# Kernel tuning notes

Hardware: AMD Instinct MI355X
Metric: run time of the kernel (lower is better)

The kernel has to match this reference:

```python
import jax, jax.numpy as jnp
import numpy as np

B, S, I, H, T = 64, 512, 300, 512, 25


def setup_inputs() -> dict:
    key = jax.random.key(0)
    ks = jax.random.split(key, 16)
    kH = 1.0 / np.sqrt(H)
    x = jax.random.normal(ks[0], (B, S, I), jnp.float32)
    lengths = jax.random.randint(ks[1], (B,), S // 2, S + 1)
    attention_mask = (jnp.arange(S)[None, :] < lengths[:, None]).astype(jnp.int32)
    raw = jax.random.randint(ks[2], (B, S), 0, T)
    labels = jnp.where(attention_mask > 0, raw, -100).astype(jnp.int32)
    u = lambda k, sh: jax.random.uniform(k, sh, jnp.float32, -kH, kH)
    return {
        'input_ids': x,
        'W_ih_f': u(ks[3], (4 * H, I)), 'W_hh_f': u(ks[4], (4 * H, H)), 'b_f': u(ks[5], (4 * H,)),
        'W_ih_b': u(ks[6], (4 * H, I)), 'W_hh_b': u(ks[7], (4 * H, H)), 'b_b': u(ks[8], (4 * H,)),
        'Wc': u(ks[9], (T, 2 * H)), 'bc': u(ks[10], (T,)),
        'crf_start': jax.random.uniform(ks[11], (T,), jnp.float32, -0.1, 0.1),
        'crf_end': jax.random.uniform(ks[12], (T,), jnp.float32, -0.1, 0.1),
        'crf_trans': jax.random.uniform(ks[13], (T, T), jnp.float32, -0.1, 0.1),
        'attention_mask': attention_mask,
        'labels': labels,
    }


def _lstm_scan(x, mask, W_ih, W_hh, b):
    # x: [B,S,I], mask: [B,S] bool. PyTorch gate order i,f,g,o. Masked steps
    # freeze (h,c) and emit zeros, matching pack_padded/pad_packed semantics.
    Bb, Ss, _ = x.shape
    Hh = W_hh.shape[1]
    pre = jnp.einsum('bsi,gi->sbg', x, W_ih) + b  # [S,B,4H] input projection
    mt = jnp.moveaxis(mask, 1, 0)                 # [S,B]

    def step(carry, xs):
        h, c = carry
        p_t, m_t = xs
        gates = p_t + h @ W_hh.T
        i, f, g, o = jnp.split(gates, 4, axis=-1)
        c_new = jax.nn.sigmoid(f) * c + jax.nn.sigmoid(i) * jnp.tanh(g)
        h_new = jax.nn.sigmoid(o) * jnp.tanh(c_new)
        m = m_t[:, None]
        return (jnp.where(m, h_new, h), jnp.where(m, c_new, c)), jnp.where(m, h_new, 0.0)

    h0 = jnp.zeros((Bb, Hh), x.dtype)
    _, ys = jax.lax.scan(step, (h0, h0), (pre, mt))
    return jnp.moveaxis(ys, 0, 1)  # [B,S,H]


def _crf_nll_token_mean(em, tags, mask, start, end, trans):
    # pytorch-crf log-likelihood with reduction='token_mean'; returns -llh.
    Bb, Ss, Tt = em.shape
    mf = mask.astype(em.dtype)
    batch = jnp.arange(Bb)
    emit = jnp.take_along_axis(em, tags[..., None], axis=2)[..., 0]  # [B,S]
    num = start[tags[:, 0]] + emit[:, 0]
    tr = trans[tags[:, :-1], tags[:, 1:]]  # [B,S-1]
    num = num + jnp.sum(mf[:, 1:] * (tr + emit[:, 1:]), axis=1)
    last_idx = jnp.sum(mask.astype(jnp.int32), axis=1) - 1
    num = num + end[tags[batch, last_idx]]

    em_t = jnp.moveaxis(em[:, 1:], 1, 0)    # [S-1,B,T]
    mk_t = jnp.moveaxis(mask[:, 1:], 1, 0)  # [S-1,B]

    def step(score, xs):
        e_t, m_t = xs
        nxt = jax.nn.logsumexp(score[:, :, None] + trans[None] + e_t[:, None, :], axis=1)
        return jnp.where(m_t[:, None], nxt, score), None

    score0 = start[None] + em[:, 0]
    score, _ = jax.lax.scan(step, score0, (em_t, mk_t))
    denom = jax.nn.logsumexp(score + end[None], axis=1)
    llh = num - denom
    return -(jnp.sum(llh) / jnp.sum(mf))


def _crf_decode(em, mask, start, end, trans):
    Bb, Ss, Tt = em.shape
    em_t = jnp.moveaxis(em[:, 1:], 1, 0)
    mk_t = jnp.moveaxis(mask[:, 1:], 1, 0)
    idT = jnp.arange(Tt)
    batch = jnp.arange(Bb)

    def step(score, xs):
        e_t, m_t = xs
        cand = score[:, :, None] + trans[None]     # [B,T,T]
        best_prev = jnp.argmax(cand, axis=1)       # [B,T]
        best = jnp.max(cand, axis=1) + e_t
        m = m_t[:, None]
        return jnp.where(m, best, score), jnp.where(m, best_prev, idT[None, :])

    score0 = start[None] + em[:, 0]
    score, hist = jax.lax.scan(step, score0, (em_t, mk_t))  # hist [S-1,B,T]
    last_tag = jnp.argmax(score + end[None], axis=1)        # [B]

    def back(tag, xs):
        h_t, m_t = xs
        tag2 = jnp.where(m_t, h_t[batch, tag], tag)
        return tag2, tag2

    _, prev_tags = jax.lax.scan(back, last_tag, (hist, mk_t), reverse=True)  # [S-1,B]
    tags = jnp.concatenate([prev_tags, last_tag[None]], axis=0)  # [S,B]
    return jnp.moveaxis(tags, 0, 1)  # [B,S]


def _forward(input_ids, W_ih_f, W_hh_f, b_f, W_ih_b, W_hh_b, b_b, Wc, bc,
             crf_start, crf_end, crf_trans, attention_mask, labels):
    mask = attention_mask > 0
    lengths = jnp.sum(attention_mask, axis=1)  # [B]
    # forward direction
    h_f = _lstm_scan(input_ids, mask, W_ih_f, W_hh_f, b_f)
    # backward direction: reverse each sequence within its valid length
    t_idx = jnp.arange(input_ids.shape[1])[None, :]
    rev = jnp.where(t_idx < lengths[:, None], lengths[:, None] - 1 - t_idx, t_idx)
    x_rev = jnp.take_along_axis(input_ids, rev[:, :, None], axis=1)
    m_rev = jnp.take_along_axis(mask, rev, axis=1)
    h_b_rev = _lstm_scan(x_rev, m_rev, W_ih_b, W_hh_b, b_b)
    h_b = jnp.take_along_axis(h_b_rev, rev[:, :, None], axis=1)  # rev is an involution on the valid prefix
    seq = jnp.concatenate([h_f, h_b], axis=-1)  # [B,S,2H]; dropout = identity (eval)
    logits = seq @ Wc.T + bc                    # [B,S,T]
    # re-pack tokens with labels >= 0 to the front (stable), as the torch loop does
    valid = labels >= 0
    order = jnp.argsort(jnp.logical_not(valid), axis=1, stable=True)
    new_logits = jnp.take_along_axis(logits, order[:, :, None], axis=1)
    new_labels = jnp.take_along_axis(labels, order, axis=1)
    pred_mask = jnp.take_along_axis(valid, order, axis=1)
    active = jnp.where(pred_mask, new_labels, 0)
    loss = _crf_nll_token_mean(new_logits, active, pred_mask, crf_start, crf_end, crf_trans)
    tags = _crf_decode(new_logits, pred_mask, crf_start, crf_end, crf_trans)
    return loss, logits, tags, pred_mask


def reference(input_ids, W_ih_f, W_hh_f, b_f, W_ih_b, W_hh_b, b_b, Wc, bc,
              crf_start, crf_end, crf_trans, attention_mask, labels):
    return _forward(input_ids, W_ih_f, W_hh_f, b_f, W_ih_b, W_hh_b, b_b, Wc, bc,
                    crf_start, crf_end, crf_trans, attention_mask, labels)
```

## Files before the change

kernel.cpp:

```cpp
#include <hip/hip_runtime.h>
#include <math.h>

#define B_ 64
#define S_ 512
#define I_ 300
#define H_ 512
#define T_ 25

typedef short bf16x8 __attribute__((ext_vector_type(8)));
typedef float f32x4  __attribute__((ext_vector_type(4)));

__host__ __device__ __forceinline__ int kmap(int l, int j) {
    return 16 * (j >> 2) + 4 * ((l >> 4) & 3) + (j & 3);
}

static constexpr size_t SZ_XBF_S = (size_t)S_ * 2 * 2 * 4 * 5 * 2 * 64 * 8;
static constexpr size_t OFS_XBF  = 0;
static constexpr size_t OFS_WHF  = OFS_XBF + SZ_XBF_S / 2;
static constexpr size_t SZ_WHF_S = (size_t)2 * 128 * 2 * 8 * 2 * 64 * 8;
static constexpr size_t OFS_WXF  = OFS_WHF + SZ_WHF_S / 2;
static constexpr size_t SZ_WXF_S = (size_t)2 * 128 * 2 * 5 * 2 * 64 * 8;
static constexpr size_t OFS_YF   = OFS_WXF + SZ_WXF_S / 2;
static constexpr size_t SZ_Y     = (size_t)S_ * H_ * B_;
static constexpr size_t OFS_YB   = OFS_YF + SZ_Y;
static constexpr size_t SZ_L     = (size_t)B_ * S_ * T_;
static constexpr size_t OFS_L1   = OFS_YB + SZ_Y;
static constexpr size_t OFS_L2   = OFS_L1 + SZ_L;
static constexpr size_t OFS_LEN  = OFS_L2 + SZ_L;
static constexpr size_t OFS_LLH  = OFS_LEN + 64;
static constexpr size_t OFS_FLG  = OFS_LLH + 64;

static constexpr size_t OFF_LOGITS = 1;
static constexpr size_t OFF_TAGS   = 1 + SZ_L;
static constexpr size_t OFF_MASK   = OFF_TAGS + (size_t)B_ * S_;

__global__ void k_lengths(const int* __restrict__ am, int* __restrict__ len) {
    int b = threadIdx.x;
    int sum = 0;
    for (int s = 0; s < S_; ++s) sum += am[b * S_ + s];
    len[b] = sum;
}

__global__ void k_zero(float* __restrict__ p, int n) {
    int idx = blockIdx.x * 256 + threadIdx.x;
    if (idx < n) p[idx] = 0.f;
}

__global__ void k_prep_hfrag(const float* __restrict__ whhf,
                             const float* __restrict__ whhb,
                             short* __restrict__ hf) {
    for (size_t idx = (size_t)blockIdx.x * 256 + threadIdx.x; idx < SZ_WHF_S;
         idx += (size_t)gridDim.x * 256) {
        int j = (int)(idx & 7); size_t t = idx >> 3;
        int l = (int)(t & 63); t >>= 6;
        int hilo = (int)(t & 1); t >>= 1;
        int kt = (int)(t & 7); t >>= 3;
        int kh = (int)(t & 1); t >>= 1;
        int ug = (int)(t & 127); t >>= 7;
        int dir = (int)t;
        int m = l & 15;
        int row = (m & 3) * H_ + ug * 4 + (m >> 2);
        int k = kh * 256 + kt * 32 + kmap(l, j);
        float w = (dir ? whhb : whhf)[(size_t)row * H_ + k];
        unsigned u32 = __float_as_uint(w);
        float hi_f = __uint_as_float(u32 & 0xffff0000u);
        hf[idx] = hilo ? (short)(__float_as_uint(w - hi_f) >> 16)
                       : (short)(u32 >> 16);
    }
}

__global__ void k_prep_xfrag(const float* __restrict__ wihf,
                             const float* __restrict__ wihb,
                             short* __restrict__ xf) {
    for (size_t idx = (size_t)blockIdx.x * 256 + threadIdx.x; idx < SZ_WXF_S;
         idx += (size_t)gridDim.x * 256) {
        int j = (int)(idx & 7); size_t t = idx >> 3;
        int l = (int)(t & 63); t >>= 6;
        int hilo = (int)(t & 1); t >>= 1;
        int kt = (int)(t % 5); t /= 5;
        int kh = (int)(t & 1); t >>= 1;
        int ug = (int)(t & 127); t >>= 7;
        int dir = (int)t;
        int m = l & 15;
        int row = (m & 3) * H_ + ug * 4 + (m >> 2);
        int k = kh * 160 + kt * 32 + kmap(l, j);
        float w = 0.f;
        if (k < I_) w = (dir ? wihb : wihf)[(size_t)row * I_ + k];
        unsigned u32 = __float_as_uint(w);
        float hi_f = __uint_as_float(u32 & 0xffff0000u);
        xf[idx] = hilo ? (short)(__float_as_uint(w - hi_f) >> 16)
                       : (short)(u32 >> 16);
    }
}

__global__ void k_prep_xb(const float* __restrict__ x, const int* __restrict__ len,
                          short* __restrict__ xb) {
    for (size_t idx = (size_t)blockIdx.x * 256 + threadIdx.x; idx < SZ_XBF_S;
         idx += (size_t)gridDim.x * 256) {
        int j = (int)(idx & 7); size_t t = idx >> 3;
        int l = (int)(t & 63); t >>= 6;
        int hilo = (int)(t & 1); t >>= 1;
        int kt = (int)(t % 5); t /= 5;
        int nt = (int)(t & 3); t >>= 2;
        int kh = (int)(t & 1); t >>= 1;
        int dir = (int)(t & 1); t >>= 1;
        int s = (int)t;
        int b = nt * 16 + (l & 15);
        int k = kh * 160 + kt * 32 + kmap(l, j);
        float v = 0.f;
        if (k < I_) {
            int src = s;
            if (dir) { int L = len[b]; src = (s < L) ? (L - 1 - s) : s; }
            v = x[((size_t)b * S_ + src) * I_ + k];
        }
        unsigned u32 = __float_as_uint(v);
        float hi_f = __uint_as_float(u32 & 0xffff0000u);
        xb[idx] = hilo ? (short)(__float_as_uint(v - hi_f) >> 16)
                       : (short)(u32 >> 16);
    }
}

__global__ __launch_bounds__(512, 2) void k_scan(
    const short* __restrict__ whf, const short* __restrict__ wxf,
    const short* __restrict__ xbf,
    float* yf, float* ybr,
    const float* __restrict__ bf, const float* __restrict__ bb,
    const int* __restrict__ len, int* __restrict__ flg)
{
    __shared__ bf16x8 hA[2 * 8 * 2 * 64];
    __shared__ bf16x8 xA[2 * 5 * 2 * 64];
    __shared__ float parts[32 * 66];
    const int dir = blockIdx.x >> 7;
    const int ug  = blockIdx.x & 127;
    const int tid = threadIdx.x;
    const int lane = tid & 63;
    const int wq = __builtin_amdgcn_readfirstlane(tid >> 6);
    const int nt = wq >> 1, kh = wq & 1;
    const int bcol = (nt << 4) + (lane & 15);

    {
        const bf16x8* whp = (const bf16x8*)whf + (size_t)(dir * 128 + ug) * 2048;
        for (int i = tid; i < 2048; i += 512) hA[i] = whp[i];
        const bf16x8* wxp = (const bf16x8*)wxf + (size_t)(dir * 128 + ug) * 1280;
        for (int i = tid; i < 1280; i += 512) xA[i] = wxp[i];
    }

    float* ybase = dir ? ybr : yf;
    int* const myflag = flg + ((size_t)(dir * 128 + ug) << 4);
    const int* const fp = flg + ((size_t)(dir * 128 + kh * 64 + lane) << 4);

    const int uF = (ug << 2) + wq;
    float c_reg = 0.f;
    float bi0 = 0.f, bi1 = 0.f, bi2 = 0.f, bi3 = 0.f;
    if (wq < 4) {
        const float* bias = dir ? bb : bf;
        bi0 = bias[uF]; bi1 = bias[H_ + uF];
        bi2 = bias[2 * H_ + uF]; bi3 = bias[3 * H_ + uF];
    }
    const int Lb = len[lane];

    int ko[8];
#pragma unroll
    for (int j = 0; j < 8; ++j) ko[j] = kmap(lane, j);

    __syncthreads();

    for (int s = 0; s < S_; ++s) {
        f32x4 d = {0.f, 0.f, 0.f, 0.f};

        {
            const bf16x8* xb = (const bf16x8*)xbf +
                ((((size_t)(s * 2 + dir) * 2 + kh) * 4 + nt) * 5) * 2 * 64;
#pragma unroll
            for (int kt = 0; kt < 5; ++kt) {
                bf16x8 b_h = xb[(kt * 2 + 0) * 64 + lane];
                bf16x8 b_l = xb[(kt * 2 + 1) * 64 + lane];
                bf16x8 a_h = xA[((kh * 5 + kt) * 2 + 0) * 64 + lane];
                bf16x8 a_l = xA[((kh * 5 + kt) * 2 + 1) * 64 + lane];
                d = __builtin_amdgcn_mfma_f32_16x16x32_bf16(a_h, b_h, d, 0, 0, 0);
                d = __builtin_amdgcn_mfma_f32_16x16x32_bf16(a_h, b_l, d, 0, 0, 0);
                d = __builtin_amdgcn_mfma_f32_16x16x32_bf16(a_l, b_h, d, 0, 0, 0);
            }
        }

        if (s) {
            for (;;) {
                int v = __hip_atomic_load(fp, __ATOMIC_RELAXED,
                                          __HIP_MEMORY_SCOPE_AGENT);
                if (__all(v >= s)) break;
                __builtin_amdgcn_s_sleep(1);
            }
        }
        asm volatile("" ::: "memory");

        if (s) {
            const float* hprev = ybase + ((size_t)(s - 1) << 15);
#pragma unroll
            for (int kt = 0; kt < 8; ++kt) {
                const int k0 = kh * 256 + kt * 32;
                float hv[8];
#pragma unroll
                for (int j = 0; j < 8; ++j)
                    hv[j] = hprev[((size_t)(k0 + ko[j]) << 6) + bcol];
                bf16x8 b_h, b_l;
#pragma unroll
                for (int j = 0; j < 8; ++j) {
                    unsigned u32 = __float_as_uint(hv[j]);
                    b_h[j] = (short)(u32 >> 16);
                    float hi_f = __uint_as_float(u32 & 0xffff0000u);
                    b_l[j] = (short)(__float_as_uint(hv[j] - hi_f) >> 16);
                }
                bf16x8 a_h = hA[((kh * 8 + kt) * 2 + 0) * 64 + lane];
                bf16x8 a_l = hA[((kh * 8 + kt) * 2 + 1) * 64 + lane];
                d = __builtin_amdgcn_mfma_f32_16x16x32_bf16(a_h, b_h, d, 0, 0, 0);
                d = __builtin_amdgcn_mfma_f32_16x16x32_bf16(a_h, b_l, d, 0, 0, 0);
                d = __builtin_amdgcn_mfma_f32_16x16x32_bf16(a_l, b_h, d, 0, 0, 0);
            }
        }

        {
            const int m0 = (lane >> 4) << 2;
#pragma unroll
            for (int r = 0; r < 4; ++r)
                parts[(kh * 16 + m0 + r) * 66 + bcol] = d[r];
        }
        __syncthreads();

        if (wq < 4) {
            const int rb = wq << 2;
            float g0 = bi0 + parts[(rb + 0) * 66 + lane] + parts[(16 + rb + 0) * 66 + lane];
            float g1 = bi1 + parts[(rb + 1) * 66 + lane] + parts[(16 + rb + 1) * 66 + lane];
            float g2 = bi2 + parts[(rb + 2) * 66 + lane] + parts[(16 + rb + 2) * 66 + lane];
            float g3 = bi3 + parts[(rb + 3) * 66 + lane] + parts[(16 + rb + 3) * 66 + lane];
            float ii = 1.f / (1.f + expf(-g0));
            float ff = 1.f / (1.f + expf(-g1));
            float gg = tanhf(g2);
            float oo = 1.f / (1.f + expf(-g3));
            float cn2 = ff * c_reg + ii * gg;
            float hn = oo * tanhf(cn2);
            c_reg = cn2;
            float yv = (s < Lb) ? hn : 0.f;
            __hip_atomic_store(&ybase[((size_t)(s * H_ + uF) << 6) + lane], yv,
                               __ATOMIC_RELAXED, __HIP_MEMORY_SCOPE_AGENT);
        }

        asm volatile("s_waitcnt vmcnt(0)" ::: "memory");
        __syncthreads();
        if (tid == 0)
            __hip_atomic_store(myflag, s + 1, __ATOMIC_RELAXED,
                               __HIP_MEMORY_SCOPE_AGENT);
    }
}

__global__ __launch_bounds__(256) void k_logits(const float* __restrict__ yf,
                                                const float* __restrict__ ybr,
                                                const float* __restrict__ wc,
                                                const float* __restrict__ bcv,
                                                float* __restrict__ L1,
                                                float* __restrict__ L2p) {
    __shared__ float smem[T_ * H_];
    int part = blockIdx.x >> 9;
    int s = blockIdx.x & 511;
    int tid = threadIdx.x;
    const float* y = part ? ybr : yf;
    float* Ldst = part ? L2p : L1;
    for (int idx = tid; idx < T_ * H_; idx += 256) {
        int t = idx >> 9;
        int h = idx & 511;
        smem[idx] = wc[(size_t)t * 1024 + part * 512 + h];
    }
    __syncthreads();
    int q = tid >> 6, b = tid & 63;
    float acc[T_];
#pragma unroll
    for (int t = 0; t < T_; ++t) acc[t] = 0.f;
    const float* yrow = y + (size_t)s * H_ * B_ + b;
    for (int h = q * 128; h < q * 128 + 128; ++h) {
        float a = yrow[(size_t)h * B_];
#pragma unroll
        for (int t = 0; t < T_; ++t) acc[t] += a * smem[t * H_ + h];
    }
    __syncthreads();
    float* pl = smem;
#pragma unroll
    for (int t = 0; t < T_; ++t) pl[(q * 64 + b) * 26 + t] = acc[t];
    __syncthreads();
    for (int idx = tid; idx < B_ * T_; idx += 256) {
        int bb2 = idx / T_;
        int t = idx - bb2 * T_;
        float v = pl[(0 * 64 + bb2) * 26 + t] + pl[(1 * 64 + bb2) * 26 + t] +
                  pl[(2 * 64 + bb2) * 26 + t] + pl[(3 * 64 + bb2) * 26 + t];
        if (!part) v += bcv[t];
        Ldst[((size_t)bb2 * S_ + s) * T_ + t] = v;
    }
}

__global__ void k_combine(const float* __restrict__ L1, const float* __restrict__ L2p,
                          const int* __restrict__ len, float* __restrict__ outlog) {
    int id = blockIdx.x * 256 + threadIdx.x;
    int b = id >> 9;
    int s = id & 511;
    int L = len[b];
    int sr = (s < L) ? (L - 1 - s) : s;
    const float* p1 = L1 + ((size_t)b * S_ + s) * T_;
    const float* p2 = L2p + ((size_t)b * S_ + sr) * T_;
    float* o = outlog + ((size_t)b * S_ + s) * T_;
#pragma unroll
    for (int t = 0; t < T_; ++t) o[t] = p1[t] + p2[t];
}

__global__ __launch_bounds__(64) void k_crf_nll(const float* __restrict__ em,
                                                const int* __restrict__ labels,
                                                const int* __restrict__ len,
                                                const float* __restrict__ cs,
                                                const float* __restrict__ ce,
                                                const float* __restrict__ ctr,
                                                float* __restrict__ llh) {
    int b = blockIdx.x, tid = threadIdx.x;
    __shared__ float tr[T_ * T_];
    __shared__ float sa[T_], sb[T_];
    for (int idx = tid; idx < T_ * T_; idx += 64) tr[idx] = ctr[idx];
    const float* e = em + (size_t)b * S_ * T_;
    int L = len[b];
    if (tid < T_) sa[tid] = cs[tid] + e[tid];
    __syncthreads();
    float* cur = sa;
    float* nx = sb;
    for (int t = 1; t < L; ++t) {
        if (tid < T_) {
            float m = -1e30f;
            for (int i = 0; i < T_; ++i) m = fmaxf(m, cur[i] + tr[i * T_ + tid]);
            float ssum = 0.f;
            for (int i = 0; i < T_; ++i) ssum += expf(cur[i] + tr[i * T_ + tid] - m);
            nx[tid] = m + logf(ssum) + e[(size_t)t * T_ + tid];
        }
        __syncthreads();
        float* tmp = cur; cur = nx; nx = tmp;
    }
    float part = 0.f;
    for (int t = tid; t < S_; t += 64) {
        if (t >= 1 && t < L) {
            int lp = labels[b * S_ + t - 1];
            int lc = labels[b * S_ + t];
            part += tr[lp * T_ + lc] + e[(size_t)t * T_ + lc];
        }
    }
    for (int off = 32; off; off >>= 1) part += __shfl_down(part, off, 64);
    if (tid == 0) {
        float m = -1e30f;
        for (int j = 0; j < T_; ++j) m = fmaxf(m, cur[j] + ce[j]);
        float ssum = 0.f;
        for (int j = 0; j < T_; ++j) ssum += expf(cur[j] + ce[j] - m);
        float denom = m + logf(ssum);
        int l0 = labels[b * S_];
        int lL = labels[b * S_ + L - 1];
        float num = cs[l0] + e[l0] + part + ce[lL];
        llh[b] = num - denom;
    }
}

__global__ void k_loss(const float* __restrict__ llh, const int* __restrict__ len,
                       float* __restrict__ out0) {
    int tid = threadIdx.x;
    float v = llh[tid];
    float n = (float)len[tid];
    for (int off = 32; off; off >>= 1) {
        v += __shfl_down(v, off, 64);
        n += __shfl_down(n, off, 64);
    }
    if (tid == 0) out0[0] = -(v / n);
}

__global__ __launch_bounds__(64) void k_viterbi(const float* __restrict__ em,
                                                const int* __restrict__ len,
                                                const float* __restrict__ cs,
                                                const float* __restrict__ ce,
                                                const float* __restrict__ ctr,
                                                float* __restrict__ otags,
                                                float* __restrict__ omask) {
    int b = blockIdx.x, tid = threadIdx.x;
    __shared__ float tr[T_ * T_];
    __shared__ float sa[T_], sb[T_];
    __shared__ unsigned char hist[(S_ - 1) * T_];
    __shared__ unsigned char tg[S_];
    for (int idx = tid; idx < T_ * T_; idx += 64) tr[idx] = ctr[idx];
    const float* e = em + (size_t)b * S_ * T_;
    int L = len[b];
    if (tid < T_) sa[tid] = cs[tid] + e[tid];
    __syncthreads();
    float* cur = sa;
    float* nx = sb;
    for (int t = 1; t < L; ++t) {
        if (tid < T_) {
            float best = -1e30f;
            int bi = 0;
            for (int i = 0; i < T_; ++i) {
                float v = cur[i] + tr[i * T_ + tid];
                if (v > best) { best = v; bi = i; }
            }
            nx[tid] = best + e[(size_t)t * T_ + tid];
            hist[(t - 1) * T_ + tid] = (unsigned char)bi;
        }
        __syncthreads();
        float* tmp = cur; cur = nx; nx = tmp;
    }
    if (tid == 0) {
        float best = -1e30f;
        int bt = 0;
        for (int j = 0; j < T_; ++j) {
            float v = cur[j] + ce[j];
            if (v > best) { best = v; bt = j; }
        }
        tg[S_ - 1] = (unsigned char)bt;
        for (int t = S_ - 2; t >= 0; --t) {
            if (t + 1 < L) bt = hist[t * T_ + bt];
            tg[t] = (unsigned char)bt;
        }
    }
    __syncthreads();
    for (int idx = tid; idx < S_; idx += 64) {
        otags[(size_t)b * S_ + idx] = (float)tg[idx];
        omask[(size_t)b * S_ + idx] = (idx < L) ? 1.f : 0.f;
    }
}

extern "C" void kernel_launch(void* const* d_in, const int* in_sizes, int n_in,
                              void* d_out, int out_size, void* d_ws, size_t ws_size,
                              hipStream_t stream) {
    const float* x    = (const float*)d_in[0];
    const float* wihf = (const float*)d_in[1];
    const float* whhf = (const float*)d_in[2];
    const float* bf   = (const float*)d_in[3];
    const float* wihb = (const float*)d_in[4];
    const float* whhb = (const float*)d_in[5];
    const float* bb   = (const float*)d_in[6];
    const float* wc   = (const float*)d_in[7];
    const float* bc   = (const float*)d_in[8];
    const float* cs   = (const float*)d_in[9];
    const float* ce   = (const float*)d_in[10];
    const float* ctr  = (const float*)d_in[11];
    const int* am     = (const int*)d_in[12];
    const int* labels = (const int*)d_in[13];

    float* ws   = (float*)d_ws;
    short* xbfr = (short*)(ws + OFS_XBF);
    short* whfr = (short*)(ws + OFS_WHF);
    short* wxfr = (short*)(ws + OFS_WXF);
    float* yf   = ws + OFS_YF;
    float* ybr  = ws + OFS_YB;
    float* L1p  = ws + OFS_L1;
    float* L2p  = ws + OFS_L2;
    int*   lenp = (int*)(ws + OFS_LEN);
    float* llhp = ws + OFS_LLH;
    int*   flgp = (int*)(ws + OFS_FLG);
    float* out  = (float*)d_out;

    k_lengths<<<1, 64, 0, stream>>>(am, lenp);
    k_prep_hfrag<<<2048, 256, 0, stream>>>(whhf, whhb, whfr);
    k_prep_xfrag<<<2048, 256, 0, stream>>>(wihf, wihb, wxfr);
    k_prep_xb<<<8192, 256, 0, stream>>>(x, lenp, xbfr);
    k_zero<<<16, 256, 0, stream>>>(ws + OFS_FLG, 2 * 128 * 16);

    {
        void* kargs[] = {
            (void*)&whfr, (void*)&wxfr, (void*)&xbfr,
            (void*)&yf, (void*)&ybr,
            (void*)&bf, (void*)&bb,
            (void*)&lenp, (void*)&flgp
        };
        hipLaunchCooperativeKernel((const void*)k_scan,
                                   dim3(256), dim3(512), kargs, 0, stream);
    }

    k_logits<<<1024, 256, 0, stream>>>(yf, ybr, wc, bc, L1p, L2p);
    k_combine<<<128, 256, 0, stream>>>(L1p, L2p, lenp, out + OFF_LOGITS);
    k_crf_nll<<<64, 64, 0, stream>>>(out + OFF_LOGITS, labels, lenp, cs, ce, ctr, llhp);
    k_loss<<<1, 64, 0, stream>>>(llhp, lenp, out);
    k_viterbi<<<64, 64, 0, stream>>>(out + OFF_LOGITS, lenp, cs, ce, ctr,
                                     out + OFF_TAGS, out + OFF_MASK);
}
```

Baseline: 3.695 ms.

## Drop the intra-block K split and sync each batch tile with per-wave flags

The recurrent scan block shrinks from 8 waves to 4. Each wave now accumulates the full K range into two accumulators and applies the LSTM gates straight from its MFMA registers. This removes the LDS partial-sum buffer and both per-step __syncthreads. Cross-block synchronization moves from per-block flags to per-wave (per batch tile) flags, so each batch tile only waits on the same tile in the other blocks. The cost is a longer serial MFMA chain per wave, less wave-level parallelism per CU, and polling twice as many flags.

```diff
diff --git a/kernel.cpp b/kernel.cpp
--- a/kernel.cpp
+++ b/kernel.cpp
@@ -120,44 +120,43 @@
     }
 }
 
-__global__ __launch_bounds__(512, 2) void k_scan(
+__global__ __launch_bounds__(256, 1) void k_scan(
     const short* __restrict__ whf, const short* __restrict__ wxf,
     const short* __restrict__ xbf,
     float* yf, float* ybr,
     const float* __restrict__ bf, const float* __restrict__ bb,
     const int* __restrict__ len, int* __restrict__ flg)
 {
-    __shared__ bf16x8 hA[2 * 8 * 2 * 64];
-    __shared__ bf16x8 xA[2 * 5 * 2 * 64];
-    __shared__ float parts[32 * 66];
+    __shared__ bf16x8 hA[16 * 2 * 64];
+    __shared__ bf16x8 xA[10 * 2 * 64];
     const int dir = blockIdx.x >> 7;
     const int ug  = blockIdx.x & 127;
     const int tid = threadIdx.x;
     const int lane = tid & 63;
-    const int wq = __builtin_amdgcn_readfirstlane(tid >> 6);
-    const int nt = wq >> 1, kh = wq & 1;
+    const int nt = __builtin_amdgcn_readfirstlane(tid >> 6);
     const int bcol = (nt << 4) + (lane & 15);
+    const int uu = lane >> 4;
+    const int unit = (ug << 2) + uu;
 
     {
         const bf16x8* whp = (const bf16x8*)whf + (size_t)(dir * 128 + ug) * 2048;
-        for (int i = tid; i < 2048; i += 512) hA[i] = whp[i];
+        for (int i = tid; i < 2048; i += 256) hA[i] = whp[i];
         const bf16x8* wxp = (const bf16x8*)wxf + (size_t)(dir * 128 + ug) * 1280;
-        for (int i = tid; i < 1280; i += 512) xA[i] = wxp[i];
+        for (int i = tid; i < 1280; i += 256) xA[i] = wxp[i];
     }
 
     float* ybase = dir ? ybr : yf;
-    int* const myflag = flg + ((size_t)(dir * 128 + ug) << 4);
-    const int* const fp = flg + ((size_t)(dir * 128 + kh * 64 + lane) << 4);
-
-    const int uF = (ug << 2) + wq;
+    int* const myflag = flg + ((size_t)(((dir * 4 + nt) * 128) + ug) << 4);
+    const int* const fp0 = flg + ((size_t)(((dir * 4 + nt) * 128) + lane) << 4);
+    const int* const fp1 = flg + ((size_t)(((dir * 4 + nt) * 128) + 64 + lane) << 4);
+
     float c_reg = 0.f;
-    float bi0 = 0.f, bi1 = 0.f, bi2 = 0.f, bi3 = 0.f;
-    if (wq < 4) {
-        const float* bias = dir ? bb : bf;
-        bi0 = bias[uF]; bi1 = bias[H_ + uF];
-        bi2 = bias[2 * H_ + uF]; bi3 = bias[3 * H_ + uF];
-    }
-    const int Lb = len[lane];
+    const float* bias = dir ? bb : bf;
+    const float bi0 = bias[unit];
+    const float bi1 = bias[H_ + unit];
+    const float bi2 = bias[2 * H_ + unit];
+    const float bi3 = bias[3 * H_ + unit];
+    const int Lb = len[bcol];
 
     int ko[8];
 #pragma unroll
@@ -166,9 +165,11 @@
     __syncthreads();
 
     for (int s = 0; s < S_; ++s) {
-        f32x4 d = {0.f, 0.f, 0.f, 0.f};
-
-        {
+        f32x4 d0 = {0.f, 0.f, 0.f, 0.f};
+        f32x4 d1 = {0.f, 0.f, 0.f, 0.f};
+
+#pragma unroll
+        for (int kh = 0; kh < 2; ++kh) {
             const bf16x8* xb = (const bf16x8*)xbf +
                 ((((size_t)(s * 2 + dir) * 2 + kh) * 4 + nt) * 5) * 2 * 64;
 #pragma unroll
@@ -177,16 +178,19 @@
                 bf16x8 b_l = xb[(kt * 2 + 1) * 64 + lane];
                 bf16x8 a_h = xA[((kh * 5 + kt) * 2 + 0) * 64 + lane];
                 bf16x8 a_l = xA[((kh * 5 + kt) * 2 + 1) * 64 + lane];
-                d = __builtin_amdgcn_mfma_f32_16x16x32_bf16(a_h, b_h, d, 0, 0, 0);
-                d = __builtin_amdgcn_mfma_f32_16x16x32_bf16(a_h, b_l, d, 0, 0, 0);
-                d = __builtin_amdgcn_mfma_f32_16x16x32_bf16(a_l, b_h, d, 0, 0, 0);
+                d0 = __builtin_amdgcn_mfma_f32_16x16x32_bf16(a_h, b_h, d0, 0, 0, 0);
+                d1 = __builtin_amdgcn_mfma_f32_16x16x32_bf16(a_h, b_l, d1, 0, 0, 0);
+                d0 = __builtin_amdgcn_mfma_f32_16x16x32_bf16(a_l, b_h, d0, 0, 0, 0);
             }
         }
 
         if (s) {
             for (;;) {
-                int v = __hip_atomic_load(fp, __ATOMIC_RELAXED,
-                                          __HIP_MEMORY_SCOPE_AGENT);
+                int v0 = __hip_atomic_load(fp0, __ATOMIC_RELAXED,
+                                           __HIP_MEMORY_SCOPE_AGENT);
+                int v1 = __hip_atomic_load(fp1, __ATOMIC_RELAXED,
+                                           __HIP_MEMORY_SCOPE_AGENT);
+                int v = v0 < v1 ? v0 : v1;
                 if (__all(v >= s)) break;
                 __builtin_amdgcn_s_sleep(1);
             }
@@ -196,8 +200,8 @@
         if (s) {
             const float* hprev = ybase + ((size_t)(s - 1) << 15);
 #pragma unroll
-            for (int kt = 0; kt < 8; ++kt) {
-                const int k0 = kh * 256 + kt * 32;
+            for (int kt2 = 0; kt2 < 16; ++kt2) {
+                const int k0 = kt2 * 32;
                 float hv[8];
 #pragma unroll
                 for (int j = 0; j < 8; ++j)
@@ -210,28 +214,19 @@
                     float hi_f = __uint_as_float(u32 & 0xffff0000u);
                     b_l[j] = (short)(__float_as_uint(hv[j] - hi_f) >> 16);
                 }
-                bf16x8 a_h = hA[((kh * 8 + kt) * 2 + 0) * 64 + lane];
-                bf16x8 a_l = hA[((kh * 8 + kt) * 2 + 1) * 64 + lane];
-                d = __builtin_amdgcn_mfma_f32_16x16x32_bf16(a_h, b_h, d, 0, 0, 0);
-                d = __builtin_amdgcn_mfma_f32_16x16x32_bf16(a_h, b_l, d, 0, 0, 0);
-                d = __builtin_amdgcn_mfma_f32_16x16x32_bf16(a_l, b_h, d, 0, 0, 0);
+                bf16x8 a_h = hA[(kt2 * 2 + 0) * 64 + lane];
+                bf16x8 a_l = hA[(kt2 * 2 + 1) * 64 + lane];
+                d0 = __builtin_amdgcn_mfma_f32_16x16x32_bf16(a_h, b_h, d0, 0, 0, 0);
+                d1 = __builtin_amdgcn_mfma_f32_16x16x32_bf16(a_h, b_l, d1, 0, 0, 0);
+                d0 = __builtin_amdgcn_mfma_f32_16x16x32_bf16(a_l, b_h, d0, 0, 0, 0);
             }
         }
 
         {
-            const int m0 = (lane >> 4) << 2;
-#pragma unroll
-            for (int r = 0; r < 4; ++r)
-                parts[(kh * 16 + m0 + r) * 66 + bcol] = d[r];
-        }
-        __syncthreads();
-
-        if (wq < 4) {
-            const int rb = wq << 2;
-            float g0 = bi0 + parts[(rb + 0) * 66 + lane] + parts[(16 + rb + 0) * 66 + lane];
-            float g1 = bi1 + parts[(rb + 1) * 66 + lane] + parts[(16 + rb + 1) * 66 + lane];
-            float g2 = bi2 + parts[(rb + 2) * 66 + lane] + parts[(16 + rb + 2) * 66 + lane];
-            float g3 = bi3 + parts[(rb + 3) * 66 + lane] + parts[(16 + rb + 3) * 66 + lane];
+            float g0 = bi0 + d0[0] + d1[0];
+            float g1 = bi1 + d0[1] + d1[1];
+            float g2 = bi2 + d0[2] + d1[2];
+            float g3 = bi3 + d0[3] + d1[3];
             float ii = 1.f / (1.f + expf(-g0));
             float ff = 1.f / (1.f + expf(-g1));
             float gg = tanhf(g2);
@@ -240,13 +235,12 @@
             float hn = oo * tanhf(cn2);
             c_reg = cn2;
             float yv = (s < Lb) ? hn : 0.f;
-            __hip_atomic_store(&ybase[((size_t)(s * H_ + uF) << 6) + lane], yv,
+            __hip_atomic_store(&ybase[((size_t)(s * H_ + unit) << 6) + bcol], yv,
                                __ATOMIC_RELAXED, __HIP_MEMORY_SCOPE_AGENT);
         }
 
         asm volatile("s_waitcnt vmcnt(0)" ::: "memory");
-        __syncthreads();
-        if (tid == 0)
+        if (lane == 0)
             __hip_atomic_store(myflag, s + 1, __ATOMIC_RELAXED,
                                __HIP_MEMORY_SCOPE_AGENT);
     }
@@ -459,7 +453,7 @@
     k_prep_hfrag<<<2048, 256, 0, stream>>>(whhf, whhb, whfr);
     k_prep_xfrag<<<2048, 256, 0, stream>>>(wihf, wihb, wxfr);
     k_prep_xb<<<8192, 256, 0, stream>>>(x, lenp, xbfr);
-    k_zero<<<16, 256, 0, stream>>>(ws + OFS_FLG, 2 * 128 * 16);
+    k_zero<<<64, 256, 0, stream>>>(ws + OFS_FLG, 2 * 4 * 128 * 16);
 
     {
         void* kargs[] = {
@@ -469,7 +463,7 @@
             (void*)&lenp, (void*)&flgp
         };
         hipLaunchCooperativeKernel((const void*)k_scan,
-                                   dim3(256), dim3(512), kargs, 0, stream);
+                                   dim3(256), dim3(256), kargs, 0, stream);
     }
 
     k_logits<<<1024, 256, 0, stream>>>(yf, ybr, wc, bc, L1p, L2p);
```

Measured after the change: 4.789 ms. 1.3x slower.

## Store hidden state as packed bf16 hi/lo in MFMA fragment layout

Applied to the files above, without the earlier changes.

The scan now writes each hidden value as a packed bf16 hi/lo pair into a buffer laid out in MFMA B-fragment order. Consumers can then load it with two vector loads per k-tile instead of eight scattered scalar loads and a per-step split. Each wave publishes its own flag right after its store, replacing the block-wide barrier and single flag. Waiters poll four flags with one dwordx4 load, and parts is double-buffered by step parity so one barrier per step suffices. MFMA accumulation is split across two accumulators to shorten dependency chains, and k_logits reconstructs the values from the hi+lo pair, which adds a small precision approximation.

```diff
diff --git a/kernel.cpp b/kernel.cpp
--- a/kernel.cpp
+++ b/kernel.cpp
@@ -9,6 +9,8 @@
 
 typedef short bf16x8 __attribute__((ext_vector_type(8)));
 typedef float f32x4  __attribute__((ext_vector_type(4)));
+typedef int   s32x4  __attribute__((ext_vector_type(4)));
+typedef unsigned u32x4 __attribute__((ext_vector_type(4)));
 
 __host__ __device__ __forceinline__ int kmap(int l, int j) {
     return 16 * (j >> 2) + 4 * ((l >> 4) & 3) + (j & 3);
@@ -20,11 +22,10 @@
 static constexpr size_t SZ_WHF_S = (size_t)2 * 128 * 2 * 8 * 2 * 64 * 8;
 static constexpr size_t OFS_WXF  = OFS_WHF + SZ_WHF_S / 2;
 static constexpr size_t SZ_WXF_S = (size_t)2 * 128 * 2 * 5 * 2 * 64 * 8;
-static constexpr size_t OFS_YF   = OFS_WXF + SZ_WXF_S / 2;
-static constexpr size_t SZ_Y     = (size_t)S_ * H_ * B_;
-static constexpr size_t OFS_YB   = OFS_YF + SZ_Y;
+static constexpr size_t OFS_HX   = OFS_WXF + SZ_WXF_S / 2;
+static constexpr size_t SZ_HX    = (size_t)S_ * 65536;
+static constexpr size_t OFS_L1   = OFS_HX + SZ_HX;
 static constexpr size_t SZ_L     = (size_t)B_ * S_ * T_;
-static constexpr size_t OFS_L1   = OFS_YB + SZ_Y;
 static constexpr size_t OFS_L2   = OFS_L1 + SZ_L;
 static constexpr size_t OFS_LEN  = OFS_L2 + SZ_L;
 static constexpr size_t OFS_LLH  = OFS_LEN + 64;
@@ -122,14 +123,13 @@
 
 __global__ __launch_bounds__(512, 2) void k_scan(
     const short* __restrict__ whf, const short* __restrict__ wxf,
-    const short* __restrict__ xbf,
-    float* yf, float* ybr,
+    const short* __restrict__ xbf, unsigned* __restrict__ hx,
     const float* __restrict__ bf, const float* __restrict__ bb,
     const int* __restrict__ len, int* __restrict__ flg)
 {
-    __shared__ bf16x8 hA[2 * 8 * 2 * 64];
-    __shared__ bf16x8 xA[2 * 5 * 2 * 64];
-    __shared__ float parts[32 * 66];
+    __shared__ bf16x8 hA[16 * 2 * 64];
+    __shared__ bf16x8 xA[10 * 2 * 64];
+    __shared__ float parts[2 * 32 * 66];
     const int dir = blockIdx.x >> 7;
     const int ug  = blockIdx.x & 127;
     const int tid = threadIdx.x;
@@ -145,9 +145,8 @@
         for (int i = tid; i < 1280; i += 512) xA[i] = wxp[i];
     }
 
-    float* ybase = dir ? ybr : yf;
-    int* const myflag = flg + ((size_t)(dir * 128 + ug) << 4);
-    const int* const fp = flg + ((size_t)(dir * 128 + kh * 64 + lane) << 4);
+    int* const flgline = flg + ((size_t)(dir * 128 + ug) << 4);
+    const int* const fpp = flg + ((size_t)(dir * 128 + (kh << 6) + lane) << 4);
 
     const int uF = (ug << 2) + wq;
     float c_reg = 0.f;
@@ -159,14 +158,16 @@
     }
     const int Lb = len[lane];
 
-    int ko[8];
-#pragma unroll
-    for (int j = 0; j < 8; ++j) ko[j] = kmap(lane, j);
+    const size_t hxoff =
+        ((size_t)(dir * 4 + (lane >> 4)) * 16 + (ug >> 3)) * 512 +
+        (size_t)((lane & 15) + ((ug & 3) << 4)) * 8 +
+        (size_t)(4 * ((ug >> 2) & 1) + wq);
 
     __syncthreads();
 
     for (int s = 0; s < S_; ++s) {
-        f32x4 d = {0.f, 0.f, 0.f, 0.f};
+        f32x4 d0 = {0.f, 0.f, 0.f, 0.f};
+        f32x4 d1 = {0.f, 0.f, 0.f, 0.f};
 
         {
             const bf16x8* xb = (const bf16x8*)xbf +
@@ -177,61 +178,68 @@
                 bf16x8 b_l = xb[(kt * 2 + 1) * 64 + lane];
                 bf16x8 a_h = xA[((kh * 5 + kt) * 2 + 0) * 64 + lane];
                 bf16x8 a_l = xA[((kh * 5 + kt) * 2 + 1) * 64 + lane];
-                d = __builtin_amdgcn_mfma_f32_16x16x32_bf16(a_h, b_h, d, 0, 0, 0);
-                d = __builtin_amdgcn_mfma_f32_16x16x32_bf16(a_h, b_l, d, 0, 0, 0);
-                d = __builtin_amdgcn_mfma_f32_16x16x32_bf16(a_l, b_h, d, 0, 0, 0);
+                d0 = __builtin_amdgcn_mfma_f32_16x16x32_bf16(a_h, b_h, d0, 0, 0, 0);
+                d1 = __builtin_amdgcn_mfma_f32_16x16x32_bf16(a_h, b_l, d1, 0, 0, 0);
+                d0 = __builtin_amdgcn_mfma_f32_16x16x32_bf16(a_l, b_h, d0, 0, 0, 0);
             }
         }
 
         if (s) {
             for (;;) {
-                int v = __hip_atomic_load(fp, __ATOMIC_RELAXED,
-                                          __HIP_MEMORY_SCOPE_AGENT);
-                if (__all(v >= s)) break;
+                s32x4 v;
+                asm volatile("global_load_dwordx4 %0, %1, off sc0 sc1\n\t"
+                             "s_waitcnt vmcnt(0)"
+                             : "=&v"(v) : "v"(fpp) : "memory");
+                int mna = v[0] < v[1] ? v[0] : v[1];
+                int mnb = v[2] < v[3] ? v[2] : v[3];
+                int mn = mna < mnb ? mna : mnb;
+                if (__all(mn >= s)) break;
                 __builtin_amdgcn_s_sleep(1);
             }
         }
         asm volatile("" ::: "memory");
 
         if (s) {
-            const float* hprev = ybase + ((size_t)(s - 1) << 15);
+            const unsigned* hxs = hx + (size_t)(s - 1) * 65536 +
+                ((size_t)(dir * 4 + nt) * 16 + (kh << 3)) * 512 + (lane << 3);
 #pragma unroll
             for (int kt = 0; kt < 8; ++kt) {
-                const int k0 = kh * 256 + kt * 32;
-                float hv[8];
-#pragma unroll
-                for (int j = 0; j < 8; ++j)
-                    hv[j] = hprev[((size_t)(k0 + ko[j]) << 6) + bcol];
-                bf16x8 b_h, b_l;
-#pragma unroll
-                for (int j = 0; j < 8; ++j) {
-                    unsigned u32 = __float_as_uint(hv[j]);
-                    b_h[j] = (short)(u32 >> 16);
-                    float hi_f = __uint_as_float(u32 & 0xffff0000u);
-                    b_l[j] = (short)(__float_as_uint(hv[j] - hi_f) >> 16);
-                }
+                const u32x4* p4 = (const u32x4*)(hxs + kt * 512);
+                u32x4 va = p4[0];
+                u32x4 vb = p4[1];
+                union { unsigned u[4]; bf16x8 v8; } bh, bl;
+                bh.u[0] = (va[0] >> 16) | (va[1] & 0xffff0000u);
+                bh.u[1] = (va[2] >> 16) | (va[3] & 0xffff0000u);
+                bh.u[2] = (vb[0] >> 16) | (vb[1] & 0xffff0000u);
+                bh.u[3] = (vb[2] >> 16) | (vb[3] & 0xffff0000u);
+                bl.u[0] = (va[0] & 0xffffu) | (va[1] << 16);
+                bl.u[1] = (va[2] & 0xffffu) | (va[3] << 16);
+                bl.u[2] = (vb[0] & 0xffffu) | (vb[1] << 16);
+                bl.u[3] = (vb[2] & 0xffffu) | (vb[3] << 16);
                 bf16x8 a_h = hA[((kh * 8 + kt) * 2 + 0) * 64 + lane];
                 bf16x8 a_l = hA[((kh * 8 + kt) * 2 + 1) * 64 + lane];
-                d = __builtin_amdgcn_mfma_f32_16x16x32_bf16(a_h, b_h, d, 0, 0, 0);
-                d = __builtin_amdgcn_mfma_f32_16x16x32_bf16(a_h, b_l, d, 0, 0, 0);
-                d = __builtin_amdgcn_mfma_f32_16x16x32_bf16(a_l, b_h, d, 0, 0, 0);
+                d0 = __builtin_amdgcn_mfma_f32_16x16x32_bf16(a_h, bh.v8, d0, 0, 0, 0);
+                d1 = __builtin_amdgcn_mfma_f32_16x16x32_bf16(a_h, bl.v8, d1, 0, 0, 0);
+                d0 = __builtin_amdgcn_mfma_f32_16x16x32_bf16(a_l, bh.v8, d0, 0, 0, 0);
             }
         }
 
+        const int par = s & 1;
         {
             const int m0 = (lane >> 4) << 2;
 #pragma unroll
             for (int r = 0; r < 4; ++r)
-                parts[(kh * 16 + m0 + r) * 66 + bcol] = d[r];
+                parts[((par << 5) + (kh << 4) + m0 + r) * 66 + bcol] = d0[r] + d1[r];
         }
         __syncthreads();
 
         if (wq < 4) {
             const int rb = wq << 2;
-            float g0 = bi0 + parts[(rb + 0) * 66 + lane] + parts[(16 + rb + 0) * 66 + lane];
-            float g1 = bi1 + parts[(rb + 1) * 66 + lane] + parts[(16 + rb + 1) * 66 + lane];
-            float g2 = bi2 + parts[(rb + 2) * 66 + lane] + parts[(16 + rb + 2) * 66 + lane];
-            float g3 = bi3 + parts[(rb + 3) * 66 + lane] + parts[(16 + rb + 3) * 66 + lane];
+            const float* pp = parts + (size_t)(par << 5) * 66;
+            float g0 = bi0 + pp[(rb + 0) * 66 + lane] + pp[(16 + rb + 0) * 66 + lane];
+            float g1 = bi1 + pp[(rb + 1) * 66 + lane] + pp[(16 + rb + 1) * 66 + lane];
+            float g2 = bi2 + pp[(rb + 2) * 66 + lane] + pp[(16 + rb + 2) * 66 + lane];
+            float g3 = bi3 + pp[(rb + 3) * 66 + lane] + pp[(16 + rb + 3) * 66 + lane];
             float ii = 1.f / (1.f + expf(-g0));
             float ff = 1.f / (1.f + expf(-g1));
             float gg = tanhf(g2);
@@ -240,20 +248,20 @@
             float hn = oo * tanhf(cn2);
             c_reg = cn2;
             float yv = (s < Lb) ? hn : 0.f;
-            __hip_atomic_store(&ybase[((size_t)(s * H_ + uF) << 6) + lane], yv,
+            unsigned u = __float_as_uint(yv);
+            unsigned hi = u & 0xffff0000u;
+            unsigned lo = __float_as_uint(yv - __uint_as_float(hi)) >> 16;
+            __hip_atomic_store(hx + (size_t)s * 65536 + hxoff, hi | lo,
                                __ATOMIC_RELAXED, __HIP_MEMORY_SCOPE_AGENT);
-        }
-
-        asm volatile("s_waitcnt vmcnt(0)" ::: "memory");
-        __syncthreads();
-        if (tid == 0)
-            __hip_atomic_store(myflag, s + 1, __ATOMIC_RELAXED,
-                               __HIP_MEMORY_SCOPE_AGENT);
-    }
-}
-
-__global__ __launch_bounds__(256) void k_logits(const float* __restrict__ yf,
-                                                const float* __restrict__ ybr,
+            asm volatile("s_waitcnt vmcnt(0)" ::: "memory");
+            if (lane == 0)
+                __hip_atomic_store(flgline + wq, s + 1, __ATOMIC_RELAXED,
+                                   __HIP_MEMORY_SCOPE_AGENT);
+        }
+    }
+}
+
+__global__ __launch_bounds__(256) void k_logits(const unsigned* __restrict__ hx,
                                                 const float* __restrict__ wc,
                                                 const float* __restrict__ bcv,
                                                 float* __restrict__ L1,
@@ -262,7 +270,6 @@
     int part = blockIdx.x >> 9;
     int s = blockIdx.x & 511;
     int tid = threadIdx.x;
-    const float* y = part ? ybr : yf;
     float* Ldst = part ? L2p : L1;
     for (int idx = tid; idx < T_ * H_; idx += 256) {
         int t = idx >> 9;
@@ -274,9 +281,15 @@
     float acc[T_];
 #pragma unroll
     for (int t = 0; t < T_; ++t) acc[t] = 0.f;
-    const float* yrow = y + (size_t)s * H_ * B_ + b;
+    const unsigned* hxs = hx + (size_t)s * 65536 +
+        (size_t)(part * 4 + (b >> 4)) * 8192;
+    const int bl8 = (b & 15) * 8;
     for (int h = q * 128; h < q * 128 + 128; ++h) {
-        float a = yrow[(size_t)h * B_];
+        int kt2 = h >> 5;
+        int lg = (h >> 2) & 3;
+        int j = ((h >> 4) & 1) * 4 + (h & 3);
+        unsigned u = hxs[(size_t)kt2 * 512 + (lg << 7) + bl8 + j];
+        float a = __uint_as_float(u & 0xffff0000u) + __uint_as_float(u << 16);
 #pragma unroll
         for (int t = 0; t < T_; ++t) acc[t] += a * smem[t * H_ + h];
     }
@@ -446,8 +459,7 @@
     short* xbfr = (short*)(ws + OFS_XBF);
     short* whfr = (short*)(ws + OFS_WHF);
     short* wxfr = (short*)(ws + OFS_WXF);
-    float* yf   = ws + OFS_YF;
-    float* ybr  = ws + OFS_YB;
+    unsigned* hxp = (unsigned*)(ws + OFS_HX);
     float* L1p  = ws + OFS_L1;
     float* L2p  = ws + OFS_L2;
     int*   lenp = (int*)(ws + OFS_LEN);
@@ -463,8 +475,7 @@
 
     {
         void* kargs[] = {
-            (void*)&whfr, (void*)&wxfr, (void*)&xbfr,
-            (void*)&yf, (void*)&ybr,
+            (void*)&whfr, (void*)&wxfr, (void*)&xbfr, (void*)&hxp,
             (void*)&bf, (void*)&bb,
             (void*)&lenp, (void*)&flgp
         };
@@ -472,7 +483,7 @@
                                    dim3(256), dim3(512), kargs, 0, stream);
     }
 
-    k_logits<<<1024, 256, 0, stream>>>(yf, ybr, wc, bc, L1p, L2p);
+    k_logits<<<1024, 256, 0, stream>>>(hxp, wc, bc, L1p, L2p);
     k_combine<<<128, 256, 0, stream>>>(L1p, L2p, lenp, out + OFF_LOGITS);
     k_crf_nll<<<64, 64, 0, stream>>>(out + OFF_LOGITS, labels, lenp, cs, ce, ctr, llhp);
     k_loss<<<1, 64, 0, stream>>>(llhp, lenp, out);
```

Result: slower. 4.195 ms (+13.5%).

## Per-wave flags and double-buffered parts to drop second block barrier in LSTM scan

Applied to the files above, without the earlier changes.

The per-step second __syncthreads and single-thread flag publish are replaced by per-wave flag words: each of the 4 gate waves publishes its own flag after its stores complete. The poller reads all four flags of a producer block with one dwordx4 load and takes their minimum. The parts buffer is double-buffered by step parity so the removed barrier does not create a write-after-read hazard. The MFMA chain is also split into two accumulators to shorten the dependent chain. This trades a block-wide barrier for more flag traffic and relies on the 4-int flag layout within each 16-int line.

```diff
diff --git a/kernel.cpp b/kernel.cpp
--- a/kernel.cpp
+++ b/kernel.cpp
@@ -9,6 +9,7 @@
 
 typedef short bf16x8 __attribute__((ext_vector_type(8)));
 typedef float f32x4  __attribute__((ext_vector_type(4)));
+typedef int   s32x4  __attribute__((ext_vector_type(4)));
 
 __host__ __device__ __forceinline__ int kmap(int l, int j) {
     return 16 * (j >> 2) + 4 * ((l >> 4) & 3) + (j & 3);
@@ -127,9 +128,9 @@
     const float* __restrict__ bf, const float* __restrict__ bb,
     const int* __restrict__ len, int* __restrict__ flg)
 {
-    __shared__ bf16x8 hA[2 * 8 * 2 * 64];
-    __shared__ bf16x8 xA[2 * 5 * 2 * 64];
-    __shared__ float parts[32 * 66];
+    __shared__ bf16x8 hA[16 * 2 * 64];
+    __shared__ bf16x8 xA[10 * 2 * 64];
+    __shared__ float parts[2 * 32 * 66];
     const int dir = blockIdx.x >> 7;
     const int ug  = blockIdx.x & 127;
     const int tid = threadIdx.x;
@@ -146,8 +147,8 @@
     }
 
     float* ybase = dir ? ybr : yf;
-    int* const myflag = flg + ((size_t)(dir * 128 + ug) << 4);
-    const int* const fp = flg + ((size_t)(dir * 128 + kh * 64 + lane) << 4);
+    int* const flgline = flg + ((size_t)(dir * 128 + ug) << 4);
+    const int* const fpp = flg + ((size_t)(dir * 128 + (kh << 6) + lane) << 4);
 
     const int uF = (ug << 2) + wq;
     float c_reg = 0.f;
@@ -166,7 +167,8 @@
     __syncthreads();
 
     for (int s = 0; s < S_; ++s) {
-        f32x4 d = {0.f, 0.f, 0.f, 0.f};
+        f32x4 d0 = {0.f, 0.f, 0.f, 0.f};
+        f32x4 d1 = {0.f, 0.f, 0.f, 0.f};
 
         {
             const bf16x8* xb = (const bf16x8*)xbf +
@@ -177,17 +179,22 @@
                 bf16x8 b_l = xb[(kt * 2 + 1) * 64 + lane];
                 bf16x8 a_h = xA[((kh * 5 + kt) * 2 + 0) * 64 + lane];
                 bf16x8 a_l = xA[((kh * 5 + kt) * 2 + 1) * 64 + lane];
-                d = __builtin_amdgcn_mfma_f32_16x16x32_bf16(a_h, b_h, d, 0, 0, 0);
-                d = __builtin_amdgcn_mfma_f32_16x16x32_bf16(a_h, b_l, d, 0, 0, 0);
-                d = __builtin_amdgcn_mfma_f32_16x16x32_bf16(a_l, b_h, d, 0, 0, 0);
+                d0 = __builtin_amdgcn_mfma_f32_16x16x32_bf16(a_h, b_h, d0, 0, 0, 0);
+                d1 = __builtin_amdgcn_mfma_f32_16x16x32_bf16(a_h, b_l, d1, 0, 0, 0);
+                d0 = __builtin_amdgcn_mfma_f32_16x16x32_bf16(a_l, b_h, d0, 0, 0, 0);
             }
         }
 
         if (s) {
             for (;;) {
-                int v = __hip_atomic_load(fp, __ATOMIC_RELAXED,
-                                          __HIP_MEMORY_SCOPE_AGENT);
-                if (__all(v >= s)) break;
+                s32x4 v;
+                asm volatile("global_load_dwordx4 %0, %1, off sc0 sc1\n\t"
+                             "s_waitcnt vmcnt(0)"
+                             : "=&v"(v) : "v"(fpp) : "memory");
+                int mna = v[0] < v[1] ? v[0] : v[1];
+                int mnb = v[2] < v[3] ? v[2] : v[3];
+                int mn = mna < mnb ? mna : mnb;
+                if (__all(mn >= s)) break;
                 __builtin_amdgcn_s_sleep(1);
             }
         }
@@ -197,7 +204,7 @@
             const float* hprev = ybase + ((size_t)(s - 1) << 15);
 #pragma unroll
             for (int kt = 0; kt < 8; ++kt) {
-                const int k0 = kh * 256 + kt * 32;
+                const int k0 = (kh << 8) + kt * 32;
                 float hv[8];
 #pragma unroll
                 for (int j = 0; j < 8; ++j)
@@ -212,26 +219,28 @@
                 }
                 bf16x8 a_h = hA[((kh * 8 + kt) * 2 + 0) * 64 + lane];
                 bf16x8 a_l = hA[((kh * 8 + kt) * 2 + 1) * 64 + lane];
-                d = __builtin_amdgcn_mfma_f32_16x16x32_bf16(a_h, b_h, d, 0, 0, 0);
-                d = __builtin_amdgcn_mfma_f32_16x16x32_bf16(a_h, b_l, d, 0, 0, 0);
-                d = __builtin_amdgcn_mfma_f32_16x16x32_bf16(a_l, b_h, d, 0, 0, 0);
+                d0 = __builtin_amdgcn_mfma_f32_16x16x32_bf16(a_h, b_h, d0, 0, 0, 0);
+                d1 = __builtin_amdgcn_mfma_f32_16x16x32_bf16(a_h, b_l, d1, 0, 0, 0);
+                d0 = __builtin_amdgcn_mfma_f32_16x16x32_bf16(a_l, b_h, d0, 0, 0, 0);
             }
         }
 
+        const int par = s & 1;
         {
             const int m0 = (lane >> 4) << 2;
 #pragma unroll
             for (int r = 0; r < 4; ++r)
-                parts[(kh * 16 + m0 + r) * 66 + bcol] = d[r];
+                parts[((par << 5) + (kh << 4) + m0 + r) * 66 + bcol] = d0[r] + d1[r];
         }
         __syncthreads();
 
         if (wq < 4) {
             const int rb = wq << 2;
-            float g0 = bi0 + parts[(rb + 0) * 66 + lane] + parts[(16 + rb + 0) * 66 + lane];
-            float g1 = bi1 + parts[(rb + 1) * 66 + lane] + parts[(16 + rb + 1) * 66 + lane];
-            float g2 = bi2 + parts[(rb + 2) * 66 + lane] + parts[(16 + rb + 2) * 66 + lane];
-            float g3 = bi3 + parts[(rb + 3) * 66 + lane] + parts[(16 + rb + 3) * 66 + lane];
+            const float* pp = parts + (size_t)(par << 5) * 66;
+            float g0 = bi0 + pp[(rb + 0) * 66 + lane] + pp[(16 + rb + 0) * 66 + lane];
+            float g1 = bi1 + pp[(rb + 1) * 66 + lane] + pp[(16 + rb + 1) * 66 + lane];
+            float g2 = bi2 + pp[(rb + 2) * 66 + lane] + pp[(16 + rb + 2) * 66 + lane];
+            float g3 = bi3 + pp[(rb + 3) * 66 + lane] + pp[(16 + rb + 3) * 66 + lane];
             float ii = 1.f / (1.f + expf(-g0));
             float ff = 1.f / (1.f + expf(-g1));
             float gg = tanhf(g2);
@@ -242,13 +251,11 @@
             float yv = (s < Lb) ? hn : 0.f;
             __hip_atomic_store(&ybase[((size_t)(s * H_ + uF) << 6) + lane], yv,
                                __ATOMIC_RELAXED, __HIP_MEMORY_SCOPE_AGENT);
-        }
-
-        asm volatile("s_waitcnt vmcnt(0)" ::: "memory");
-        __syncthreads();
-        if (tid == 0)
-            __hip_atomic_store(myflag, s + 1, __ATOMIC_RELAXED,
-                               __HIP_MEMORY_SCOPE_AGENT);
+            asm volatile("s_waitcnt vmcnt(0)" ::: "memory");
+            if (lane == 0)
+                __hip_atomic_store(flgline + wq, s + 1, __ATOMIC_RELAXED,
+                                   __HIP_MEMORY_SCOPE_AGENT);
+        }
     }
 }
 
```

New measurement: 4.464 ms. 1.21x slower.
